# Optimization experiments

Hardware: AMD Instinct MI355X
Metric: run time of the kernel (lower is better)

The kernel has to match this reference:

```python
import jax, jax.numpy as jnp
import numpy as np

KS = 3          # ksize
PAD = 1         # (ksize-1)//2 * dilation, dilation=1

def setup_inputs() -> dict:
    key = jax.random.key(0)
    k1, k2, k3, k4 = jax.random.split(key, 4)
    B, NI, C, H, W = 4, 64, 64, 256, 256
    features = jax.random.normal(k1, (B, NI, H, W), jnp.float32)
    inpt = jax.random.normal(k2, (B, C, H, W), jnp.float32)
    # get_filter: Conv2d(ni, ksize**2, 3, padding=1 reflect, stride=1)
    w = jax.random.normal(k3, (KS * KS, NI, 3, 3), jnp.float32) * 0.05
    b = jax.random.normal(k4, (KS * KS,), jnp.float32) * 0.01
    return {"features": features, "inpt": inpt, "w": w, "b": b}

def reference(features, inpt, w, b):
    # 1) predict per-pixel filters: 3x3 conv with reflect padding
    fpad = jnp.pad(features, ((0, 0), (0, 0), (1, 1), (1, 1)), mode="reflect")
    ff = jax.lax.conv_general_dilated(
        fpad, w, window_strides=(1, 1), padding="VALID",
        dimension_numbers=("NCHW", "OIHW", "NCHW"),
    ) + b[None, :, None, None]                       # [B, 9, H, W]
    ff = jax.nn.softmax(ff, axis=1)                  # softmax over the 9 taps

    # 2) apply per-pixel filter to inpt (shared across channels)
    B, C, H, W = inpt.shape
    ipad = jnp.pad(inpt, ((0, 0), (0, 0), (PAD, PAD), (PAD, PAD)), mode="reflect")
    # unfold: taps in row-major (ki, kj) order, matching torch nn.Unfold
    patches = jnp.stack(
        [ipad[:, :, i:i + H, j:j + W] for i in range(KS) for j in range(KS)],
        axis=2,
    )                                                # [B, C, 9, H, W]
    # out[b,c,h,w] = sum_k patches[b,c,k,h,w] * ff[b,k,h,w]
    return jnp.einsum("bckhw,bkhw->bchw", patches, ff)
```

## Files before the change

kernel.cpp:

```cpp
#include <hip/hip_runtime.h>
#include <math.h>

#define BB 4
#define NIC 64
#define CC 64
#define HH 256
#define WW 256
#define HW (HH * WW)

#define SRW 68
#define BUFW 272

__device__ __forceinline__ int refl(int i, int n) {
    i = (i < 0) ? -i : i;
    return (i >= n) ? (2 * n - 2 - i) : i;
}

__global__ __launch_bounds__(512) void pff_wave4(
    const float* __restrict__ features,
    const float* __restrict__ inpt,
    const float* __restrict__ wgt,
    const float* __restrict__ bias,
    float* __restrict__ out)
{
    __shared__ float stage[8][2 * BUFW];
    __shared__ float part[4][9][128];

    const int tid  = threadIdx.x;
    const int wv   = __builtin_amdgcn_readfirstlane(tid >> 6);
    const int q    = wv >> 1;
    const int tr   = wv & 1;
    const int l    = tid & 63;
    const int p    = tid & 127;
    const int W0 = blockIdx.x * 64;
    const int H0 = blockIdx.y * 4;
    const int b  = blockIdx.z;

    int goff[5], loff[5];
    #pragma unroll
    for (int t = 0; t < 5; ++t) {
        const int e = (t < 4) ? (l + 64 * t) : (256 + (l & 7));
        const int row = e / 66, col = e - row * 66;
        loff[t] = row * SRW + col;
        goff[t] = refl(H0 + 2 * tr - 1 + row, HH) * WW + refl(W0 - 1 + col, WW);
    }
    const bool do5 = (l < 8);

    float accA[9], accB[9];
    #pragma unroll
    for (int k = 0; k < 9; ++k) { accA[k] = 0.f; accB[k] = 0.f; }

    float* sb = &stage[wv][0];

    const float* fb = features + (size_t)b * NIC * HW + (size_t)q * 16 * HW;
    float r0 = fb[goff[0]], r1 = fb[goff[1]], r2 = fb[goff[2]], r3 = fb[goff[3]];
    float r4 = do5 ? fb[goff[4]] : 0.f;

    for (int ni = 0; ni < 16; ++ni) {
        float* bw = sb + (ni & 1) * BUFW;
        bw[loff[0]] = r0; bw[loff[1]] = r1; bw[loff[2]] = r2; bw[loff[3]] = r3;
        if (do5) bw[loff[4]] = r4;
        if (ni < 15) {
            const float* fn = fb + (size_t)(ni + 1) * HW;
            r0 = fn[goff[0]]; r1 = fn[goff[1]]; r2 = fn[goff[2]]; r3 = fn[goff[3]];
            if (do5) r4 = fn[goff[4]];
        }

        float f[12];
        #pragma unroll
        for (int rr = 0; rr < 4; ++rr) {
            const float* br = bw + rr * SRW + l;
            f[rr * 3 + 0] = br[0];
            f[rr * 3 + 1] = br[1];
            f[rr * 3 + 2] = br[2];
        }

        const float* wn = wgt + (q * 16 + ni) * 9;
        #pragma unroll
        for (int k = 0; k < 9; ++k) {
            const float* wk = wn + k * (NIC * 9);
            const float w0 = wk[0], w1 = wk[1], w2 = wk[2];
            const float w3 = wk[3], w4 = wk[4], w5 = wk[5];
            const float w6 = wk[6], w7 = wk[7], w8 = wk[8];
            accA[k] = fmaf(f[0],  w0, accA[k]);
            accB[k] = fmaf(f[3],  w0, accB[k]);
            accA[k] = fmaf(f[1],  w1, accA[k]);
            accB[k] = fmaf(f[4],  w1, accB[k]);
            accA[k] = fmaf(f[2],  w2, accA[k]);
            accB[k] = fmaf(f[5],  w2, accB[k]);
            accA[k] = fmaf(f[3],  w3, accA[k]);
            accB[k] = fmaf(f[6],  w3, accB[k]);
            accA[k] = fmaf(f[4],  w4, accA[k]);
            accB[k] = fmaf(f[7],  w4, accB[k]);
            accA[k] = fmaf(f[5],  w5, accA[k]);
            accB[k] = fmaf(f[8],  w5, accB[k]);
            accA[k] = fmaf(f[6],  w6, accA[k]);
            accB[k] = fmaf(f[9],  w6, accB[k]);
            accA[k] = fmaf(f[7],  w7, accA[k]);
            accB[k] = fmaf(f[10], w7, accB[k]);
            accA[k] = fmaf(f[8],  w8, accA[k]);
            accB[k] = fmaf(f[11], w8, accB[k]);
        }
    }

    const float* ib = inpt + (size_t)b * CC * HW + (size_t)q * 16 * HW;
    r0 = ib[goff[0]]; r1 = ib[goff[1]]; r2 = ib[goff[2]]; r3 = ib[goff[3]];
    if (do5) r4 = ib[goff[4]];

    #pragma unroll
    for (int k = 0; k < 9; ++k) part[q][k][p] = accA[k];
    __syncthreads();
    #pragma unroll
    for (int k = 0; k < 9; ++k)
        accA[k] = part[0][k][p] + part[1][k][p] + part[2][k][p] + part[3][k][p]
                + bias[k];
    __syncthreads();
    #pragma unroll
    for (int k = 0; k < 9; ++k) part[q][k][p] = accB[k];
    __syncthreads();
    #pragma unroll
    for (int k = 0; k < 9; ++k)
        accB[k] = part[0][k][p] + part[1][k][p] + part[2][k][p] + part[3][k][p]
                + bias[k];

    {
        float m = accA[0];
        #pragma unroll
        for (int k = 1; k < 9; ++k) m = fmaxf(m, accA[k]);
        float s = 0.f;
        #pragma unroll
        for (int k = 0; k < 9; ++k) { accA[k] = __expf(accA[k] - m); s += accA[k]; }
        const float inv = 1.f / s;
        #pragma unroll
        for (int k = 0; k < 9; ++k) accA[k] *= inv;
    }
    {
        float m = accB[0];
        #pragma unroll
        for (int k = 1; k < 9; ++k) m = fmaxf(m, accB[k]);
        float s = 0.f;
        #pragma unroll
        for (int k = 0; k < 9; ++k) { accB[k] = __expf(accB[k] - m); s += accB[k]; }
        const float inv = 1.f / s;
        #pragma unroll
        for (int k = 0; k < 9; ++k) accB[k] *= inv;
    }

    float* ob = out + (size_t)b * CC * HW + (size_t)q * 16 * HW;
    const int oA = (H0 + 2 * tr) * WW + W0 + l;
    const int oB = oA + WW;

    for (int ch = 0; ch < 16; ++ch) {
        float* bw = sb + (ch & 1) * BUFW;
        bw[loff[0]] = r0; bw[loff[1]] = r1; bw[loff[2]] = r2; bw[loff[3]] = r3;
        if (do5) bw[loff[4]] = r4;
        if (ch < 15) {
            const float* in2 = ib + (size_t)(ch + 1) * HW;
            r0 = in2[goff[0]]; r1 = in2[goff[1]]; r2 = in2[goff[2]]; r3 = in2[goff[3]];
            if (do5) r4 = in2[goff[4]];
        }

        float f[12];
        #pragma unroll
        for (int rr = 0; rr < 4; ++rr) {
            const float* br = bw + rr * SRW + l;
            f[rr * 3 + 0] = br[0];
            f[rr * 3 + 1] = br[1];
            f[rr * 3 + 2] = br[2];
        }

        float vA = accA[0] * f[0];
        float vB = accB[0] * f[3];
        vA = fmaf(accA[1], f[1],  vA);  vB = fmaf(accB[1], f[4],  vB);
        vA = fmaf(accA[2], f[2],  vA);  vB = fmaf(accB[2], f[5],  vB);
        vA = fmaf(accA[3], f[3],  vA);  vB = fmaf(accB[3], f[6],  vB);
        vA = fmaf(accA[4], f[4],  vA);  vB = fmaf(accB[4], f[7],  vB);
        vA = fmaf(accA[5], f[5],  vA);  vB = fmaf(accB[5], f[8],  vB);
        vA = fmaf(accA[6], f[6],  vA);  vB = fmaf(accB[6], f[9],  vB);
        vA = fmaf(accA[7], f[7],  vA);  vB = fmaf(accB[7], f[10], vB);
        vA = fmaf(accA[8], f[8],  vA);  vB = fmaf(accB[8], f[11], vB);
        ob[(size_t)ch * HW + oA] = vA;
        ob[(size_t)ch * HW + oB] = vB;
    }
}

extern "C" void kernel_launch(void* const* d_in, const int* in_sizes, int n_in,
                              void* d_out, int out_size, void* d_ws, size_t ws_size,
                              hipStream_t stream) {
    const float* features = (const float*)d_in[0];
    const float* inpt     = (const float*)d_in[1];
    const float* wgt      = (const float*)d_in[2];
    const float* bias     = (const float*)d_in[3];
    float* out            = (float*)d_out;

    dim3 grid(WW / 64, HH / 4, BB);
    dim3 block(512);
    pff_wave4<<<grid, block, 0, stream>>>(features, inpt, wgt, bias, out);
}
```

Baseline: 70.39 us.

## Split into bf16 MFMA filter-conv kernel and separate apply kernel via workspace

```diff
diff --git a/kernel.cpp b/kernel.cpp
--- a/kernel.cpp
+++ b/kernel.cpp
@@ -11,9 +11,211 @@
 #define SRW 68
 #define BUFW 272
 
+typedef short sh8 __attribute__((ext_vector_type(8)));
+typedef float f32x4 __attribute__((ext_vector_type(4)));
+
 __device__ __forceinline__ int refl(int i, int n) {
     i = (i < 0) ? -i : i;
     return (i >= n) ? (2 * n - 2 - i) : i;
+}
+__device__ __forceinline__ unsigned short f2bf(float v) {
+    unsigned int x = __builtin_bit_cast(unsigned int, v);
+    return (unsigned short)((x + 0x7FFFu + ((x >> 16) & 1u)) >> 16);
+}
+
+__global__ void pff_prep(const float* __restrict__ wgt, uint4* __restrict__ wtab) {
+    int e = blockIdx.x * 256 + threadIdx.x;
+    if (e >= 1152) return;
+    const int c = e >> 6, l = e & 63;
+    const int p = c / 9, s = c - p * 9;
+    const int tap = l & 15, kg = l >> 4;
+    unsigned short h[8];
+    #pragma unroll
+    for (int j = 0; j < 8; ++j) {
+        const int ni = 32 * p + 8 * kg + j;
+        const float v = (tap <= 8) ? wgt[tap * 576 + ni * 9 + s] : 0.f;
+        h[j] = f2bf(v);
+    }
+    uint4 o;
+    o.x = h[0] | ((unsigned)h[1] << 16);
+    o.y = h[2] | ((unsigned)h[3] << 16);
+    o.z = h[4] | ((unsigned)h[5] << 16);
+    o.w = h[6] | ((unsigned)h[7] << 16);
+    wtab[e] = o;
+}
+
+__global__ __launch_bounds__(512) void pff_conv(
+    const float* __restrict__ features,
+    const float* __restrict__ bias,
+    const uint4* __restrict__ wtab,
+    float* __restrict__ ff)
+{
+    __shared__ unsigned short FT[10 * 34 * 34];
+
+    const int tid = threadIdx.x;
+    const int wv  = __builtin_amdgcn_readfirstlane(tid >> 6);
+    const int l   = tid & 63;
+    const int pxl = l & 15, kg = l >> 4;
+    const int W0 = blockIdx.x * 32, H0 = blockIdx.y * 8, b = blockIdx.z;
+
+    int stg_g[11], stg_l[11];
+    #pragma unroll
+    for (int i = 0; i < 11; ++i) {
+        const int flat = tid + 512 * i;
+        const int nip = flat / 340;
+        const int rc  = flat - nip * 340;
+        const int r   = rc / 34, c2 = rc - r * 34;
+        stg_l[i] = (flat < 5440) ? ((r * 34 + c2) * 34 + 2 * nip) : -1;
+        stg_g[i] = refl(H0 - 1 + r, HH) * WW + refl(W0 - 1 + c2, WW)
+                 + 2 * nip * HW;
+    }
+
+    f32x4 acc[2];
+    acc[0] = (f32x4){0.f, 0.f, 0.f, 0.f};
+    acc[1] = (f32x4){0.f, 0.f, 0.f, 0.f};
+
+    #pragma unroll
+    for (int p = 0; p < 2; ++p) {
+        uint4 wf[9];
+        #pragma unroll
+        for (int s = 0; s < 9; ++s) wf[s] = wtab[(p * 9 + s) * 64 + l];
+
+        const float* fp0 = features + ((size_t)b * NIC + 32 * p) * HW;
+        #pragma unroll
+        for (int i = 0; i < 11; ++i) {
+            if (stg_l[i] >= 0) {
+                const float* fp = fp0 + stg_g[i];
+                const unsigned pk = f2bf(fp[0]) | ((unsigned)f2bf(fp[HW]) << 16);
+                *(unsigned*)&FT[stg_l[i]] = pk;
+            }
+        }
+        __syncthreads();
+
+        #pragma unroll
+        for (int g = 0; g < 2; ++g) {
+            #pragma unroll
+            for (int s = 0; s < 9; ++s) {
+                const int di = s / 3, dj = s - di * 3;
+                const unsigned* q = (const unsigned*)
+                    &FT[((wv + di) * 34 + pxl + 16 * g + dj) * 34 + kg * 8];
+                uint4 bw;
+                bw.x = q[0]; bw.y = q[1]; bw.z = q[2]; bw.w = q[3];
+                acc[g] = __builtin_amdgcn_mfma_f32_16x16x32_bf16(
+                    __builtin_bit_cast(sh8, wf[s]),
+                    __builtin_bit_cast(sh8, bw), acc[g], 0, 0, 0);
+            }
+        }
+        if (p == 0) __syncthreads();
+    }
+
+    float bv4[4];
+    #pragma unroll
+    for (int j = 0; j < 4; ++j) {
+        const int tap = 4 * kg + j;
+        bv4[j] = bias[tap <= 8 ? tap : 8];
+    }
+    #pragma unroll
+    for (int g = 0; g < 2; ++g) {
+        float lg[4]; bool val[4];
+        #pragma unroll
+        for (int j = 0; j < 4; ++j) {
+            const int tap = 4 * kg + j;
+            val[j] = (tap <= 8);
+            lg[j] = acc[g][j] + bv4[j];
+        }
+        float ml = -3e38f;
+        #pragma unroll
+        for (int j = 0; j < 4; ++j) ml = fmaxf(ml, val[j] ? lg[j] : -3e38f);
+        float m = fmaxf(ml, __shfl_xor(ml, 16));
+        m = fmaxf(m, __shfl_xor(m, 32));
+        float e[4], sl = 0.f;
+        #pragma unroll
+        for (int j = 0; j < 4; ++j) { e[j] = val[j] ? __expf(lg[j] - m) : 0.f; sl += e[j]; }
+        float s = sl + __shfl_xor(sl, 16);
+        s += __shfl_xor(s, 32);
+        const float inv = 1.f / s;
+        #pragma unroll
+        for (int j = 0; j < 4; ++j) {
+            const int tap = 4 * kg + j;
+            if (val[j])
+                ff[(size_t)(b * 9 + tap) * HW + (H0 + wv) * WW + W0 + 16 * g + pxl]
+                    = e[j] * inv;
+        }
+    }
+}
+
+__global__ __launch_bounds__(512) void pff_apply(
+    const float* __restrict__ inpt,
+    const float* __restrict__ ff,
+    float* __restrict__ out)
+{
+    __shared__ float stage[8][2 * BUFW];
+
+    const int tid = threadIdx.x;
+    const int wv  = __builtin_amdgcn_readfirstlane(tid >> 6);
+    const int q   = wv >> 1;
+    const int tr  = wv & 1;
+    const int l   = tid & 63;
+    const int W0 = blockIdx.x * 64;
+    const int H0 = blockIdx.y * 4;
+    const int b  = blockIdx.z;
+
+    int goff[5], loff[5];
+    #pragma unroll
+    for (int t = 0; t < 5; ++t) {
+        const int e = (t < 4) ? (l + 64 * t) : (256 + (l & 7));
+        const int row = e / 66, col = e - row * 66;
+        loff[t] = row * SRW + col;
+        goff[t] = refl(H0 + 2 * tr - 1 + row, HH) * WW + refl(W0 - 1 + col, WW);
+    }
+    const bool do5 = (l < 8);
+
+    const int oA = (H0 + 2 * tr) * WW + W0 + l;
+    const int oB = oA + WW;
+    const float* ffb = ff + (size_t)b * 9 * HW;
+    float ffA[9], ffB[9];
+    #pragma unroll
+    for (int k = 0; k < 9; ++k) { ffA[k] = ffb[k * HW + oA]; ffB[k] = ffb[k * HW + oB]; }
+
+    const float* ip = inpt + ((size_t)b * CC + q * 16) * HW;
+    float* ob       = out  + ((size_t)b * CC + q * 16) * HW;
+    float* sb = &stage[wv][0];
+
+    float r0 = ip[goff[0]], r1 = ip[goff[1]], r2 = ip[goff[2]], r3 = ip[goff[3]];
+    float r4 = do5 ? ip[goff[4]] : 0.f;
+
+    for (int ch = 0; ch < 16; ++ch) {
+        float* bw = sb + (ch & 1) * BUFW;
+        bw[loff[0]] = r0; bw[loff[1]] = r1; bw[loff[2]] = r2; bw[loff[3]] = r3;
+        if (do5) bw[loff[4]] = r4;
+        if (ch < 15) {
+            const float* in2 = ip + (size_t)(ch + 1) * HW;
+            r0 = in2[goff[0]]; r1 = in2[goff[1]]; r2 = in2[goff[2]]; r3 = in2[goff[3]];
+            if (do5) r4 = in2[goff[4]];
+        }
+
+        float f[12];
+        #pragma unroll
+        for (int rr = 0; rr < 4; ++rr) {
+            const float* br = bw + rr * SRW + l;
+            f[rr * 3 + 0] = br[0];
+            f[rr * 3 + 1] = br[1];
+            f[rr * 3 + 2] = br[2];
+        }
+
+        float vA = ffA[0] * f[0];
+        float vB = ffB[0] * f[3];
+        vA = fmaf(ffA[1], f[1],  vA);  vB = fmaf(ffB[1], f[4],  vB);
+        vA = fmaf(ffA[2], f[2],  vA);  vB = fmaf(ffB[2], f[5],  vB);
+        vA = fmaf(ffA[3], f[3],  vA);  vB = fmaf(ffB[3], f[6],  vB);
+        vA = fmaf(ffA[4], f[4],  vA);  vB = fmaf(ffB[4], f[7],  vB);
+        vA = fmaf(ffA[5], f[5],  vA);  vB = fmaf(ffB[5], f[8],  vB);
+        vA = fmaf(ffA[6], f[6],  vA);  vB = fmaf(ffB[6], f[9],  vB);
+        vA = fmaf(ffA[7], f[7],  vA);  vB = fmaf(ffB[7], f[10], vB);
+        vA = fmaf(ffA[8], f[8],  vA);  vB = fmaf(ffB[8], f[11], vB);
+        ob[(size_t)ch * HW + oA] = vA;
+        ob[(size_t)ch * HW + oB] = vB;
+    }
 }
 
 __global__ __launch_bounds__(512) void pff_wave4(
@@ -51,7 +253,6 @@
     for (int k = 0; k < 9; ++k) { accA[k] = 0.f; accB[k] = 0.f; }
 
     float* sb = &stage[wv][0];
-
     const float* fb = features + (size_t)b * NIC * HW + (size_t)q * 16 * HW;
     float r0 = fb[goff[0]], r1 = fb[goff[1]], r2 = fb[goff[2]], r3 = fb[goff[3]];
     float r4 = do5 ? fb[goff[4]] : 0.f;
@@ -65,7 +266,6 @@
             r0 = fn[goff[0]]; r1 = fn[goff[1]]; r2 = fn[goff[2]]; r3 = fn[goff[3]];
             if (do5) r4 = fn[goff[4]];
         }
-
         float f[12];
         #pragma unroll
         for (int rr = 0; rr < 4; ++rr) {
@@ -74,7 +274,6 @@
             f[rr * 3 + 1] = br[1];
             f[rr * 3 + 2] = br[2];
         }
-
         const float* wn = wgt + (q * 16 + ni) * 9;
         #pragma unroll
         for (int k = 0; k < 9; ++k) {
@@ -112,16 +311,14 @@
     __syncthreads();
     #pragma unroll
     for (int k = 0; k < 9; ++k)
-        accA[k] = part[0][k][p] + part[1][k][p] + part[2][k][p] + part[3][k][p]
-                + bias[k];
+        accA[k] = part[0][k][p] + part[1][k][p] + part[2][k][p] + part[3][k][p] + bias[k];
     __syncthreads();
     #pragma unroll
     for (int k = 0; k < 9; ++k) part[q][k][p] = accB[k];
     __syncthreads();
     #pragma unroll
     for (int k = 0; k < 9; ++k)
-        accB[k] = part[0][k][p] + part[1][k][p] + part[2][k][p] + part[3][k][p]
-                + bias[k];
+        accB[k] = part[0][k][p] + part[1][k][p] + part[2][k][p] + part[3][k][p] + bias[k];
 
     {
         float m = accA[0];
@@ -149,7 +346,6 @@
     float* ob = out + (size_t)b * CC * HW + (size_t)q * 16 * HW;
     const int oA = (H0 + 2 * tr) * WW + W0 + l;
     const int oB = oA + WW;
-
     for (int ch = 0; ch < 16; ++ch) {
         float* bw = sb + (ch & 1) * BUFW;
         bw[loff[0]] = r0; bw[loff[1]] = r1; bw[loff[2]] = r2; bw[loff[3]] = r3;
@@ -159,7 +355,6 @@
             r0 = in2[goff[0]]; r1 = in2[goff[1]]; r2 = in2[goff[2]]; r3 = in2[goff[3]];
             if (do5) r4 = in2[goff[4]];
         }
-
         float f[12];
         #pragma unroll
         for (int rr = 0; rr < 4; ++rr) {
@@ -168,7 +363,6 @@
             f[rr * 3 + 1] = br[1];
             f[rr * 3 + 2] = br[2];
         }
-
         float vA = accA[0] * f[0];
         float vB = accB[0] * f[3];
         vA = fmaf(accA[1], f[1],  vA);  vB = fmaf(accB[1], f[4],  vB);
@@ -193,7 +387,23 @@
     const float* bias     = (const float*)d_in[3];
     float* out            = (float*)d_out;
 
-    dim3 grid(WW / 64, HH / 4, BB);
-    dim3 block(512);
-    pff_wave4<<<grid, block, 0, stream>>>(features, inpt, wgt, bias, out);
-}
+    const size_t WTAB_B = 18432;
+    const size_t FF_B   = (size_t)BB * 9 * HW * 4;
+
+    if (ws_size >= WTAB_B + FF_B) {
+        uint4* wtab = (uint4*)d_ws;
+        float* ff   = (float*)((char*)d_ws + WTAB_B);
+
+        pff_prep<<<dim3(5), dim3(256), 0, stream>>>(wgt, wtab);
+
+        dim3 g1(WW / 32, HH / 8, BB);
+        pff_conv<<<g1, dim3(512), 0, stream>>>(features, bias, wtab, ff);
+
+        dim3 g2(WW / 64, HH / 4, BB);
+        pff_apply<<<g2, dim3(512), 0, stream>>>(inpt, ff, out);
+    } else {
+        dim3 grid(WW / 64, HH / 4, BB);
+        dim3 block(512);
+        pff_wave4<<<grid, block, 0, stream>>>(features, inpt, wgt, bias, out);
+    }
+}
```

Measured after the change: 84.57 us. 1.2x slower.
